# Kernel tuning notes

Measured on AMD Instinct MI355X. Metric: run time of the kernel, lower is better.

## Reference

```python
import jax, jax.numpy as jnp
import numpy as np
import math

N_HEADS = 16

def _ln(x, g, b, eps=1e-5):
    m = jnp.mean(x, axis=-1, keepdims=True)
    v = jnp.var(x, axis=-1, keepdims=True)
    return (x - m) * jax.lax.rsqrt(v + eps) * g + b

def _block(x, ln1_g, ln1_b, ln2_g, ln2_b, wqkv, wo, w1, w2):
    b, k, d = x.shape
    dh = d // N_HEADS
    h = _ln(x, ln1_g, ln1_b)
    qkv = (h @ wqkv).reshape(b, k, 3, N_HEADS, dh)
    q, kk, v = qkv[:, :, 0], qkv[:, :, 1], qkv[:, :, 2]
    scores = jnp.einsum('bqhd,bkhd->bhqk', q, kk) / math.sqrt(dh)
    attn = jax.nn.softmax(scores, axis=-1)
    o = jnp.einsum('bhqk,bkhd->bqhd', attn, v).reshape(b, k, d) @ wo
    x = x + o
    h2 = _ln(x, ln2_g, ln2_b)
    return x + jax.nn.gelu(h2 @ w1) @ w2

def setup_inputs() -> dict:
    key = jax.random.key(0)
    ks = jax.random.split(key, 6)
    b, s, d, dff = 4, 4096, 1024, 4096
    sc = 0.02
    return {
        'x': jax.random.normal(ks[0], (b, s, d), jnp.float32),
        'router_w': jax.random.normal(ks[1], (d,), jnp.float32) * sc,
        'ln1_g': jnp.ones((d,), jnp.float32),
        'ln1_b': jnp.zeros((d,), jnp.float32),
        'ln2_g': jnp.ones((d,), jnp.float32),
        'ln2_b': jnp.zeros((d,), jnp.float32),
        'wqkv': jax.random.normal(ks[2], (d, 3 * d), jnp.float32) * sc,
        'wo': jax.random.normal(ks[3], (d, d), jnp.float32) * sc,
        'w1': jax.random.normal(ks[4], (d, dff), jnp.float32) * sc,
        'w2': jax.random.normal(ks[5], (dff, d), jnp.float32) * sc,
    }

def reference(x, router_w, ln1_g, ln1_b, ln2_g, ln2_b, wqkv, wo, w1, w2):
    b, s, d = x.shape
    K = s // 2  # top_k = int(s * capacity_factor), capacity_factor = 0.5
    logits = x @ router_w                      # [b, s]
    w, idx = jax.lax.top_k(logits, K)          # [b, K]
    order = jnp.argsort(idx, axis=1)           # sort selected tokens by position
    sel = jnp.take_along_axis(idx, order, axis=1)          # [b, K] sorted indices
    fx = jnp.take_along_axis(x, sel[..., None], axis=1)    # gather routed tokens [b, K, d]
    xo = _block(fx, ln1_g, ln1_b, ln2_g, ln2_b, wqkv, wo, w1, w2)
    rw = jnp.take_along_axis(jax.nn.softmax(w, axis=1), order, axis=1)[..., None]  # [b, K, 1]
    batch_idx = jnp.arange(b)[:, None]
    out = x.at[batch_idx, sel].add(rw * xo)    # softmax-weighted scatter-add
    return out
```

## Files before the change

kernel.cpp:

```cpp
#include <hip/hip_runtime.h>
#include <hip/hip_bf16.h>
#include <stdint.h>

typedef __hip_bfloat16 bf16;
typedef __attribute__((ext_vector_type(8))) short short8;
typedef __attribute__((ext_vector_type(4))) float f32x4;
typedef __attribute__((ext_vector_type(2))) unsigned uint2v;
typedef __attribute__((ext_vector_type(4))) unsigned uint4v;
typedef __attribute__((ext_vector_type(4))) unsigned short ushort4v;

#define B_   4
#define S_   4096
#define D_   1024
#define KSEL 2048
#define DFF  4096
#define NH   16
#define DH   64

static __device__ __forceinline__ void load_lds16(const void* g, void* l) {
  __builtin_amdgcn_global_load_lds((const __attribute__((address_space(1))) void*)g,
                                   (__attribute__((address_space(3))) void*)l,
                                   16, 0, 0);
}

static __device__ __forceinline__ short8 scale8(short8 v, float s) {
  short8 r;
#pragma unroll
  for (int i = 0; i < 8; ++i) {
    unsigned u = ((unsigned)(unsigned short)v[i]) << 16;
    float f = __uint_as_float(u) * s;
    bf16 o = __float2bfloat16(f);
    short t;
    __builtin_memcpy(&t, &o, 2);
    r[i] = t;
  }
  return r;
}

static __device__ __forceinline__ unsigned cvt_pk_bf16(float lo, float hi) {
  unsigned r;
  asm("v_cvt_pk_bf16_f32 %0, %1, %2" : "=v"(r) : "v"(lo), "v"(hi));
  return r;
}

static __device__ __forceinline__ void pl32_swap(unsigned &a, unsigned &b) {
#if __has_builtin(__builtin_amdgcn_permlane32_swap)
  uint2v r = __builtin_amdgcn_permlane32_swap(a, b, false, false);
  a = r[0]; b = r[1];
#else
  asm("v_permlane32_swap_b32 %0, %1" : "+v"(a), "+v"(b));
#endif
}

static __device__ __forceinline__ void pl16_swap(unsigned &a, unsigned &b) {
#if __has_builtin(__builtin_amdgcn_permlane16_swap)
  uint2v r = __builtin_amdgcn_permlane16_swap(a, b, false, false);
  a = r[0]; b = r[1];
#else
  asm("v_permlane16_swap_b32 %0, %1" : "+v"(a), "+v"(b));
#endif
}

__global__ __launch_bounds__(256)
void copy_router(const float* __restrict__ x, const float* __restrict__ rwts,
                 float* __restrict__ out, float* __restrict__ logits)
{
  int s = blockIdx.x, b = blockIdx.y;
  int tid = threadIdx.x;
  const float4* row = (const float4*)(x + ((size_t)b * S_ + s) * D_);
  float4 v = row[tid];
  ((float4*)(out + ((size_t)b * S_ + s) * D_))[tid] = v;
  float4 rv = ((const float4*)rwts)[tid];
  float p = v.x * rv.x + v.y * rv.y + v.z * rv.z + v.w * rv.w;
  for (int off = 32; off; off >>= 1) p += __shfl_down(p, off, 64);
  __shared__ float wsum[4];
  if ((tid & 63) == 0) wsum[tid >> 6] = p;
  __syncthreads();
  if (tid == 0) logits[(size_t)b * S_ + s] = wsum[0] + wsum[1] + wsum[2] + wsum[3];
}

__global__ __launch_bounds__(1024)
void topk_kernel(const float* __restrict__ logits,
                 int* __restrict__ sel, float* __restrict__ rw)
{
  __shared__ float lg[4096];
  __shared__ unsigned long long keys[4096];
  __shared__ unsigned char flags[4096];
  __shared__ float wsum[16];
  __shared__ int wtot[16];
  __shared__ int woff[17];

  int b = blockIdx.x, tid = threadIdx.x;
  const float* L = logits + (size_t)b * S_;
  for (int i = tid; i < 4096; i += 1024) {
    float v = L[i];
    lg[i] = v;
    unsigned u = __float_as_uint(v);
    u = (u & 0x80000000u) ? ~u : (u | 0x80000000u);
    u = ~u;
    keys[i] = ((unsigned long long)u << 32) | (unsigned)i;
  }
  __syncthreads();
  for (int k = 2; k <= 4096; k <<= 1) {
    for (int j = k >> 1; j > 0; j >>= 1) {
      for (int t = tid; t < 4096; t += 1024) {
        int ixj = t ^ j;
        if (ixj > t) {
          bool up = ((t & k) == 0);
          unsigned long long a = keys[t], c = keys[ixj];
          if ((a > c) == up) { keys[t] = c; keys[ixj] = a; }
        }
      }
      __syncthreads();
    }
  }
  for (int i = tid; i < 4096; i += 1024) flags[i] = 0;
  __syncthreads();
  for (int i = tid; i < KSEL; i += 1024) flags[(int)(keys[i] & 0xFFFFFFFFu)] = 1;
  __syncthreads();
  float m = lg[(int)(keys[0] & 0xFFFFFFFFu)];
  float part = 0.f;
  for (int i = tid; i < KSEL; i += 1024) part += __expf(lg[(int)(keys[i] & 0xFFFFFFFFu)] - m);
  for (int off = 32; off; off >>= 1) part += __shfl_down(part, off, 64);
  if ((tid & 63) == 0) wsum[tid >> 6] = part;
  __syncthreads();
  if (tid == 0) { float t = 0; for (int w = 0; w < 16; ++w) t += wsum[w]; wsum[0] = t; }
  __syncthreads();
  float inv = 1.0f / wsum[0];
  int base = tid * 4;
  int f0 = flags[base], f1 = flags[base + 1], f2 = flags[base + 2], f3 = flags[base + 3];
  int mysum = f0 + f1 + f2 + f3;
  int incl = mysum;
  int lane = tid & 63;
  for (int off = 1; off < 64; off <<= 1) {
    int t = __shfl_up(incl, off, 64);
    if (lane >= off) incl += t;
  }
  if (lane == 63) wtot[tid >> 6] = incl;
  __syncthreads();
  if (tid == 0) { int sacc = 0; for (int w = 0; w < 16; ++w) { woff[w] = sacc; sacc += wtot[w]; } woff[16] = sacc; }
  __syncthreads();
  int p = woff[tid >> 6] + incl - mysum;
  int fl[4] = { f0, f1, f2, f3 };
  for (int q = 0; q < 4; ++q) {
    if (fl[q]) {
      int idx = base + q;
      sel[b * KSEL + p] = idx;
      rw[b * KSEL + p] = __expf(lg[idx] - m) * inv;
      p++;
    }
  }
}

__global__ __launch_bounds__(256)
void ln_kernel(const float* __restrict__ in, const float* __restrict__ x,
               const int* __restrict__ sel,
               const float* __restrict__ g, const float* __restrict__ beta,
               bf16* __restrict__ out, int gather)
{
  int r = blockIdx.x;
  int tid = threadIdx.x;
  const float* src;
  if (gather) {
    int b = r >> 11, t = r & 2047;
    src = x + ((size_t)b * S_ + sel[b * KSEL + t]) * D_;
  } else {
    src = in + (size_t)r * D_;
  }
  float4 v = ((const float4*)src)[tid];
  float s = v.x + v.y + v.z + v.w;
  float sq = v.x * v.x + v.y * v.y + v.z * v.z + v.w * v.w;
  for (int off = 32; off; off >>= 1) { s += __shfl_down(s, off, 64); sq += __shfl_down(sq, off, 64); }
  __shared__ float wsA[4], wsB[4];
  if ((tid & 63) == 0) { wsA[tid >> 6] = s; wsB[tid >> 6] = sq; }
  __syncthreads();
  float stot = wsA[0] + wsA[1] + wsA[2] + wsA[3];
  float sqt  = wsB[0] + wsB[1] + wsB[2] + wsB[3];
  float mean = stot * (1.f / 1024.f);
  float var  = sqt * (1.f / 1024.f) - mean * mean;
  float rs = rsqrtf(var + 1e-5f);
  float4 gv = ((const float4*)g)[tid];
  float4 bv = ((const float4*)beta)[tid];
  bf16* o = out + (size_t)r * D_ + tid * 4;
  o[0] = __float2bfloat16((v.x - mean) * rs * gv.x + bv.x);
  o[1] = __float2bfloat16((v.y - mean) * rs * gv.y + bv.y);
  o[2] = __float2bfloat16((v.z - mean) * rs * gv.z + bv.z);
  o[3] = __float2bfloat16((v.w - mean) * rs * gv.w + bv.w);
}

__global__ __launch_bounds__(256)
void wtrans(const float* __restrict__ in, bf16* __restrict__ out, int K, int N)
{
  __shared__ float tile[32][33];
  int n0 = blockIdx.x * 32, k0 = blockIdx.y * 32;
  int r = threadIdx.x >> 5, c = threadIdx.x & 31;
#pragma unroll
  for (int i = 0; i < 4; ++i)
    tile[r + 8 * i][c] = in[(size_t)(k0 + r + 8 * i) * N + n0 + c];
  __syncthreads();
#pragma unroll
  for (int i = 0; i < 4; ++i)
    out[(size_t)(n0 + r + 8 * i) * K + k0 + c] = __float2bfloat16(tile[c][r + 8 * i]);
}

__global__ __launch_bounds__(256)
void vt_transpose(const bf16* __restrict__ qkv, bf16* __restrict__ vt)
{
  __shared__ bf16 tile[32][33];
  int bh = blockIdx.z;
  int d0 = blockIdx.y * 32;
  int t0 = blockIdx.x * 32;
  int b = bh >> 4, h = bh & 15;
  int r = threadIdx.x >> 5, c = threadIdx.x & 31;
#pragma unroll
  for (int i = 0; i < 4; ++i) {
    int t = t0 + r + 8 * i;
    tile[r + 8 * i][c] = qkv[(size_t)(b * KSEL + t) * 3072 + 2048 + h * 64 + d0 + c];
  }
  __syncthreads();
#pragma unroll
  for (int i = 0; i < 4; ++i) {
    int d = d0 + r + 8 * i;
    vt[((size_t)bh * 64 + d) * KSEL + t0 + c] = tile[c][r + 8 * i];
  }
}

template<int EPI, int TN>
__global__ __launch_bounds__(256)
void gemm_bt(const bf16* __restrict__ A, const bf16* __restrict__ Bt,
             float* __restrict__ Cf, bf16* __restrict__ Cb,
             int M, int N, int K,
             const float* __restrict__ xin, const int* __restrict__ sel,
             const float* __restrict__ rw, const float* __restrict__ x1,
             float* __restrict__ outp)
{
  constexpr int NT = TN / 32;
  constexpr int WN = TN / 2;
  __shared__ bf16 As[128 * 64];
  __shared__ bf16 Bs[TN * 64];
  const int tid = threadIdx.x;
  const int wid = tid >> 6;
  const int lane = tid & 63;
  const int l15 = lane & 15;
  const int quad = lane >> 4;
  const int wm = wid >> 1, wn = wid & 1;
  const int bm = blockIdx.x * 128;
  const int bn = blockIdx.y * TN;

  const int srow = lane >> 3;
  const int sgrp = (lane & 7) ^ srow;

  f32x4 acc[4][NT] = {};

  for (int k0 = 0; k0 < K; k0 += 64) {
#pragma unroll
    for (int c2 = 0; c2 < 4; ++c2) {
      int c = wid * 4 + c2;
      const bf16* ga = A + (size_t)(bm + c * 8 + srow) * K + (k0 + sgrp * 8);
      load_lds16(ga, &As[c * 512]);
    }
#pragma unroll
    for (int c2 = 0; c2 < TN / 32; ++c2) {
      int c = wid * (TN / 32) + c2;
      const bf16* gb = Bt + (size_t)(bn + c * 8 + srow) * K + (k0 + sgrp * 8);
      load_lds16(gb, &Bs[c * 512]);
    }
    __syncthreads();
#pragma unroll
    for (int ks = 0; ks < 2; ++ks) {
      short8 af[4], bfv[NT];
#pragma unroll
      for (int mt = 0; mt < 4; ++mt) {
        int row = wm * 64 + mt * 16 + l15;
        int cg = (ks * 4 + quad) ^ (row & 7);
        af[mt] = *(const short8*)&As[row * 64 + cg * 8];
      }
#pragma unroll
      for (int nt = 0; nt < NT; ++nt) {
        int row = wn * WN + nt * 16 + l15;
        int cg = (ks * 4 + quad) ^ (row & 7);
        bfv[nt] = *(const short8*)&Bs[row * 64 + cg * 8];
      }
#pragma unroll
      for (int mt = 0; mt < 4; ++mt)
#pragma unroll
        for (int nt = 0; nt < NT; ++nt)
          acc[mt][nt] = __builtin_amdgcn_mfma_f32_16x16x32_bf16(af[mt], bfv[nt], acc[mt][nt], 0, 0, 0);
    }
    __syncthreads();
  }

#pragma unroll
  for (int mt = 0; mt < 4; ++mt) {
#pragma unroll
    for (int r = 0; r < 4; ++r) {
      int gm = bm + wm * 64 + mt * 16 + quad * 4 + r;
      int bb = gm >> 11, tt = gm & 2047;
      int sr = 0; float rwv = 0.f;
      if (EPI == 1 || EPI == 3) sr = sel[bb * KSEL + tt];
      if (EPI == 3) rwv = rw[bb * KSEL + tt];
#pragma unroll
      for (int nt = 0; nt < NT; ++nt) {
        int gn = bn + wn * WN + nt * 16 + l15;
        float v = acc[mt][nt][r];
        if (EPI == 0) {
          Cb[(size_t)gm * N + gn] = __float2bfloat16(v);
        } else if (EPI == 1) {
          float xv = xin[((size_t)bb * S_ + sr) * D_ + gn];
          Cf[(size_t)gm * N + gn] = xv + v;
        } else if (EPI == 2) {
          float u = v;
          float cc = 0.7978845608028654f * (u + 0.044715f * u * u * u);
          float e = __expf(2.f * cc);
          float th = 1.f - 2.f / (e + 1.f);
          Cb[(size_t)gm * N + gn] = __float2bfloat16(0.5f * u * (1.f + th));
        } else {
          float v2 = rwv * (x1[(size_t)gm * D_ + gn] + v);
          outp[((size_t)bb * S_ + sr) * D_ + gn] += v2;
        }
      }
    }
  }
}

__global__ __launch_bounds__(256)
void flash_kernel(const bf16* __restrict__ qkv, const bf16* __restrict__ vt,
                  bf16* __restrict__ attn_o)
{
  __shared__ bf16 Ks[128 * 64];
  __shared__ bf16 Vs[64 * 128];
  int qt = blockIdx.x, h = blockIdx.y, b = blockIdx.z;
  int tid = threadIdx.x, wid = tid >> 6, lane = tid & 63;
  int l15 = lane & 15, quad = lane >> 4;
  int q0 = qt * 128 + wid * 32;

  const int srowK = lane >> 3, sgK = lane & 7;
  const int srowV = lane >> 4, sgV = lane & 15;

  short8 qf[2][2];
#pragma unroll
  for (int mt = 0; mt < 2; ++mt)
#pragma unroll
    for (int ks = 0; ks < 2; ++ks) {
      const bf16* p = qkv + (size_t)(b * KSEL + q0 + mt * 16 + l15) * 3072 + h * 64 + ks * 32 + quad * 8;
      qf[mt][ks] = scale8(*(const short8*)p, 0.125f * 1.44269504f);
    }

  f32x4 acc_ot[2][4] = {};
  float lsum[2] = {};

  const bf16* Vg = vt + (size_t)(b * NH + h) * 64 * KSEL;

  for (int kt = 0; kt < KSEL / 128; ++kt) {
    int tok0 = b * KSEL + kt * 128;
    __syncthreads();
#pragma unroll
    for (int i = 0; i < 4; ++i) {
      int c = wid * 4 + i;
      const bf16* ga = qkv + (size_t)(tok0 + c * 8 + srowK) * 3072 + 1024 + h * 64 + ((sgK ^ srowK) * 8);
      load_lds16(ga, &Ks[c * 512]);
      int vr = c * 4 + srowV;
      const bf16* gv = Vg + (size_t)vr * KSEL + kt * 128 + ((sgV ^ (vr & 7)) * 8);
      load_lds16(gv, &Vs[c * 512]);
    }
    __syncthreads();

#pragma unroll
    for (int ks4 = 0; ks4 < 4; ++ks4) {
      f32x4 s[2][2] = {};
#pragma unroll
      for (int u = 0; u < 2; ++u) {
        int row = (ks4 * 2 + u) * 16 + l15;
#pragma unroll
        for (int ks = 0; ks < 2; ++ks) {
          int g = (ks * 4 + quad) ^ (row & 7);
          short8 kf = *(const short8*)&Ks[row * 64 + g * 8];
#pragma unroll
          for (int mt = 0; mt < 2; ++mt)
            s[mt][u] = __builtin_amdgcn_mfma_f32_16x16x32_bf16(kf, qf[mt][ks], s[mt][u], 0, 0, 0);
        }
      }
      short8 pfrag[2];
#pragma unroll
      for (int mt = 0; mt < 2; ++mt) {
        float pA[4], pB[4];
#pragma unroll
        for (int r = 0; r < 4; ++r) {
          pA[r] = __builtin_amdgcn_exp2f(s[mt][0][r]);
          pB[r] = __builtin_amdgcn_exp2f(s[mt][1][r]);
          lsum[mt] += pA[r] + pB[r];
        }
        unsigned A0 = cvt_pk_bf16(pA[0], pA[1]);
        unsigned A1 = cvt_pk_bf16(pA[2], pA[3]);
        unsigned B0 = cvt_pk_bf16(pB[0], pB[1]);
        unsigned B1 = cvt_pk_bf16(pB[2], pB[3]);
        pl32_swap(A0, B0); pl16_swap(A0, B0);
        pl32_swap(A1, B1); pl16_swap(A1, B1);
        uint4v w; w[0] = A0; w[1] = A1; w[2] = B0; w[3] = B1;
        pfrag[mt] = __builtin_bit_cast(short8, w);
      }
#pragma unroll
      for (int dt = 0; dt < 4; ++dt) {
        int row = dt * 16 + l15;
        int g = (ks4 * 4 + quad) ^ (row & 7);
        short8 vf = *(const short8*)&Vs[row * 128 + g * 8];
#pragma unroll
        for (int mt = 0; mt < 2; ++mt)
          acc_ot[mt][dt] = __builtin_amdgcn_mfma_f32_16x16x32_bf16(vf, pfrag[mt], acc_ot[mt][dt], 0, 0, 0);
      }
    }
  }
#pragma unroll
  for (int mt = 0; mt < 2; ++mt) {
    float l = lsum[mt];
    l += __shfl_xor(l, 16, 64);
    l += __shfl_xor(l, 32, 64);
    float invl = 1.0f / l;
#pragma unroll
    for (int dt = 0; dt < 4; ++dt) {
      ushort4v o;
#pragma unroll
      for (int r = 0; r < 4; ++r) {
        bf16 t = __float2bfloat16(acc_ot[mt][dt][r] * invl);
        unsigned short us;
        __builtin_memcpy(&us, &t, 2);
        o[r] = us;
      }
      *(ushort4v*)(attn_o + (size_t)(b * KSEL + q0 + mt * 16 + l15) * D_ + h * 64 + dt * 16 + quad * 4) = o;
    }
  }
}

extern "C" void kernel_launch(void* const* d_in, const int* in_sizes, int n_in,
                              void* d_out, int out_size, void* d_ws, size_t ws_size,
                              hipStream_t stream)
{
  const float* x      = (const float*)d_in[0];
  const float* router = (const float*)d_in[1];
  const float* ln1g   = (const float*)d_in[2];
  const float* ln1b   = (const float*)d_in[3];
  const float* ln2g   = (const float*)d_in[4];
  const float* ln2b   = (const float*)d_in[5];
  const float* wqkv   = (const float*)d_in[6];
  const float* wo     = (const float*)d_in[7];
  const float* w1     = (const float*)d_in[8];
  const float* w2     = (const float*)d_in[9];
  float* out = (float*)d_out;
  char* ws = (char*)d_ws;

  float* logits = (float*)(ws + 0);
  int*   sel    = (int*)  (ws + 65536);
  float* rw     = (float*)(ws + 98304);
  bf16* wqkvT   = (bf16*) (ws + 131072);
  bf16* woT     = (bf16*) (ws + 6422528);
  bf16* w1T     = (bf16*) (ws + 8519680);
  bf16* w2T     = (bf16*) (ws + 16908288);
  bf16* regA    = (bf16*) (ws + 25296896);
  bf16* regB    = (bf16*) (ws + 42074112);
  bf16* vtb     = (bf16*) (ws + 42074112 + 50331648);
  float* x1     = (float*)(ws + 109182976);

  copy_router<<<dim3(S_, B_), 256, 0, stream>>>(x, router, out, logits);
  topk_kernel<<<B_, 1024, 0, stream>>>(logits, sel, rw);

  wtrans<<<dim3(3072 / 32, 1024 / 32), 256, 0, stream>>>(wqkv, wqkvT, 1024, 3072);
  wtrans<<<dim3(1024 / 32, 1024 / 32), 256, 0, stream>>>(wo,   woT,   1024, 1024);
  wtrans<<<dim3(4096 / 32, 1024 / 32), 256, 0, stream>>>(w1,   w1T,   1024, 4096);
  wtrans<<<dim3(1024 / 32, 4096 / 32), 256, 0, stream>>>(w2,   w2T,   4096, 1024);

  ln_kernel<<<B_ * KSEL, 256, 0, stream>>>(nullptr, x, sel, ln1g, ln1b, regA, 1);

  gemm_bt<0, 128><<<dim3(64, 24), 256, 0, stream>>>(regA, wqkvT, nullptr, regB, 8192, 3072, 1024,
                                                    nullptr, nullptr, nullptr, nullptr, nullptr);
  vt_transpose<<<dim3(KSEL / 32, 2, B_ * NH), 256, 0, stream>>>(regB, vtb);
  flash_kernel<<<dim3(KSEL / 128, NH, B_), 256, 0, stream>>>(regB, vtb, regA);

  gemm_bt<1, 64><<<dim3(64, 16), 256, 0, stream>>>(regA, woT, x1, nullptr, 8192, 1024, 1024,
                                                   x, sel, nullptr, nullptr, nullptr);
  ln_kernel<<<B_ * KSEL, 256, 0, stream>>>(x1, nullptr, nullptr, ln2g, ln2b, regA, 0);
  gemm_bt<2, 128><<<dim3(64, 32), 256, 0, stream>>>(regA, w1T, nullptr, regB, 8192, 4096, 1024,
                                                    nullptr, nullptr, nullptr, nullptr, nullptr);
  gemm_bt<3, 64><<<dim3(64, 16), 256, 0, stream>>>(regB, w2T, nullptr, nullptr, 8192, 1024, 4096,
                                                   nullptr, sel, rw, x1, out);
}
```

Before: 645.7 us.

## Radix-select top-k, double-buffer flash K/V tiles, widen output GEMM tiles

The top-k kernel swaps its full 4096-element bitonic sort for a 32-pass bitwise radix threshold search over register-held keys. Ties at the threshold are broken by position through a prefix scan, and the max is computed by reduction. The flash attention kernel double-buffers its K/V LDS tiles so the next tile's global-to-LDS load is issued before the current tile is computed. The Wo and W2 GEMMs move to 128-wide N tiles with half the grid. Costs are twice the LDS in flash, fewer blocks for the output GEMMs, and tie ordering that differs from the sort-based selection.

```diff
diff --git a/kernel.cpp b/kernel.cpp
--- a/kernel.cpp
+++ b/kernel.cpp
@@ -83,70 +83,91 @@
 void topk_kernel(const float* __restrict__ logits,
                  int* __restrict__ sel, float* __restrict__ rw)
 {
-  __shared__ float lg[4096];
-  __shared__ unsigned long long keys[4096];
-  __shared__ unsigned char flags[4096];
-  __shared__ float wsum[16];
-  __shared__ int wtot[16];
-  __shared__ int woff[17];
+  __shared__ int   wredi[16];
+  __shared__ float wredf[16];
+  __shared__ int   woff[17];
 
   int b = blockIdx.x, tid = threadIdx.x;
+  int lane = tid & 63, wv = tid >> 6;
   const float* L = logits + (size_t)b * S_;
-  for (int i = tid; i < 4096; i += 1024) {
-    float v = L[i];
-    lg[i] = v;
-    unsigned u = __float_as_uint(v);
-    u = (u & 0x80000000u) ? ~u : (u | 0x80000000u);
-    u = ~u;
-    keys[i] = ((unsigned long long)u << 32) | (unsigned)i;
-  }
-  __syncthreads();
-  for (int k = 2; k <= 4096; k <<= 1) {
-    for (int j = k >> 1; j > 0; j >>= 1) {
-      for (int t = tid; t < 4096; t += 1024) {
-        int ixj = t ^ j;
-        if (ixj > t) {
-          bool up = ((t & k) == 0);
-          unsigned long long a = keys[t], c = keys[ixj];
-          if ((a > c) == up) { keys[t] = c; keys[ixj] = a; }
-        }
-      }
-      __syncthreads();
-    }
-  }
-  for (int i = tid; i < 4096; i += 1024) flags[i] = 0;
-  __syncthreads();
-  for (int i = tid; i < KSEL; i += 1024) flags[(int)(keys[i] & 0xFFFFFFFFu)] = 1;
-  __syncthreads();
-  float m = lg[(int)(keys[0] & 0xFFFFFFFFu)];
+  int base = tid * 4;
+  float4 v = ((const float4*)L)[tid];
+  unsigned k0, k1, k2, k3;
+  {
+    unsigned u;
+    u = __float_as_uint(v.x); k0 = (u & 0x80000000u) ? ~u : (u | 0x80000000u);
+    u = __float_as_uint(v.y); k1 = (u & 0x80000000u) ? ~u : (u | 0x80000000u);
+    u = __float_as_uint(v.z); k2 = (u & 0x80000000u) ? ~u : (u | 0x80000000u);
+    u = __float_as_uint(v.w); k3 = (u & 0x80000000u) ? ~u : (u | 0x80000000u);
+  }
+  float mx = fmaxf(fmaxf(v.x, v.y), fmaxf(v.z, v.w));
+  for (int off = 32; off; off >>= 1) mx = fmaxf(mx, __shfl_xor(mx, off, 64));
+  if (lane == 0) wredf[wv] = mx;
+  __syncthreads();
+  float m = wredf[0];
+  for (int w = 1; w < 16; ++w) m = fmaxf(m, wredf[w]);
+
+  unsigned T = 0;
+  for (int bit = 31; bit >= 0; --bit) {
+    unsigned cand = T | (1u << bit);
+    int c = (int)(k0 >= cand) + (int)(k1 >= cand) + (int)(k2 >= cand) + (int)(k3 >= cand);
+    for (int off = 32; off; off >>= 1) c += __shfl_xor(c, off, 64);
+    __syncthreads();
+    if (lane == 0) wredi[wv] = c;
+    __syncthreads();
+    int tot = 0;
+    for (int w = 0; w < 16; ++w) tot += wredi[w];
+    if (tot >= KSEL) T = cand;
+  }
+  int cg = (int)(k0 > T) + (int)(k1 > T) + (int)(k2 > T) + (int)(k3 > T);
+  for (int off = 32; off; off >>= 1) cg += __shfl_xor(cg, off, 64);
+  __syncthreads();
+  if (lane == 0) wredi[wv] = cg;
+  __syncthreads();
+  int n_gt = 0;
+  for (int w = 0; w < 16; ++w) n_gt += wredi[w];
+  int need = KSEL - n_gt;
+  int e0 = (k0 == T), e1 = (k1 == T), e2 = (k2 == T), e3 = (k3 == T);
+  int esum = e0 + e1 + e2 + e3;
+  int eincl = esum;
+  for (int off = 1; off < 64; off <<= 1) { int t = __shfl_up(eincl, off, 64); if (lane >= off) eincl += t; }
+  __syncthreads();
+  if (lane == 63) wredi[wv] = eincl;
+  __syncthreads();
+  int ebase = 0;
+  for (int w = 0; w < wv; ++w) ebase += wredi[w];
+  int ep = ebase + eincl - esum;
+  int f0 = (k0 > T) || (e0 && ep < need); ep += e0;
+  int f1 = (k1 > T) || (e1 && ep < need); ep += e1;
+  int f2 = (k2 > T) || (e2 && ep < need); ep += e2;
+  int f3 = (k3 > T) || (e3 && ep < need); ep += e3;
   float part = 0.f;
-  for (int i = tid; i < KSEL; i += 1024) part += __expf(lg[(int)(keys[i] & 0xFFFFFFFFu)] - m);
-  for (int off = 32; off; off >>= 1) part += __shfl_down(part, off, 64);
-  if ((tid & 63) == 0) wsum[tid >> 6] = part;
-  __syncthreads();
-  if (tid == 0) { float t = 0; for (int w = 0; w < 16; ++w) t += wsum[w]; wsum[0] = t; }
-  __syncthreads();
-  float inv = 1.0f / wsum[0];
-  int base = tid * 4;
-  int f0 = flags[base], f1 = flags[base + 1], f2 = flags[base + 2], f3 = flags[base + 3];
+  if (f0) part += __expf(v.x - m);
+  if (f1) part += __expf(v.y - m);
+  if (f2) part += __expf(v.z - m);
+  if (f3) part += __expf(v.w - m);
+  for (int off = 32; off; off >>= 1) part += __shfl_xor(part, off, 64);
+  __syncthreads();
+  if (lane == 0) wredf[wv] = part;
+  __syncthreads();
+  float tot = 0.f;
+  for (int w = 0; w < 16; ++w) tot += wredf[w];
+  float inv = 1.0f / tot;
   int mysum = f0 + f1 + f2 + f3;
   int incl = mysum;
-  int lane = tid & 63;
-  for (int off = 1; off < 64; off <<= 1) {
-    int t = __shfl_up(incl, off, 64);
-    if (lane >= off) incl += t;
-  }
-  if (lane == 63) wtot[tid >> 6] = incl;
-  __syncthreads();
-  if (tid == 0) { int sacc = 0; for (int w = 0; w < 16; ++w) { woff[w] = sacc; sacc += wtot[w]; } woff[16] = sacc; }
-  __syncthreads();
-  int p = woff[tid >> 6] + incl - mysum;
-  int fl[4] = { f0, f1, f2, f3 };
+  for (int off = 1; off < 64; off <<= 1) { int t = __shfl_up(incl, off, 64); if (lane >= off) incl += t; }
+  __syncthreads();
+  if (lane == 63) wredi[wv] = incl;
+  __syncthreads();
+  if (tid == 0) { int s = 0; for (int w = 0; w < 16; ++w) { woff[w] = s; s += wredi[w]; } woff[16] = s; }
+  __syncthreads();
+  int p = woff[wv] + incl - mysum;
+  float vv[4] = { v.x, v.y, v.z, v.w };
+  int ff[4] = { f0, f1, f2, f3 };
   for (int q = 0; q < 4; ++q) {
-    if (fl[q]) {
-      int idx = base + q;
-      sel[b * KSEL + p] = idx;
-      rw[b * KSEL + p] = __expf(lg[idx] - m) * inv;
+    if (ff[q]) {
+      sel[b * KSEL + p] = base + q;
+      rw[b * KSEL + p] = __expf(vv[q] - m) * inv;
       p++;
     }
   }
@@ -327,8 +348,8 @@
 void flash_kernel(const bf16* __restrict__ qkv, const bf16* __restrict__ vt,
                   bf16* __restrict__ attn_o)
 {
-  __shared__ bf16 Ks[128 * 64];
-  __shared__ bf16 Vs[64 * 128];
+  __shared__ bf16 Ks[2][128 * 64];
+  __shared__ bf16 Vs[2][64 * 128];
   int qt = blockIdx.x, h = blockIdx.y, b = blockIdx.z;
   int tid = threadIdx.x, wid = tid >> 6, lane = tid & 63;
   int l15 = lane & 15, quad = lane >> 4;
@@ -351,19 +372,34 @@
 
   const bf16* Vg = vt + (size_t)(b * NH + h) * 64 * KSEL;
 
-  for (int kt = 0; kt < KSEL / 128; ++kt) {
-    int tok0 = b * KSEL + kt * 128;
-    __syncthreads();
+  {
+    int tok0 = b * KSEL;
 #pragma unroll
     for (int i = 0; i < 4; ++i) {
       int c = wid * 4 + i;
       const bf16* ga = qkv + (size_t)(tok0 + c * 8 + srowK) * 3072 + 1024 + h * 64 + ((sgK ^ srowK) * 8);
-      load_lds16(ga, &Ks[c * 512]);
+      load_lds16(ga, &Ks[0][c * 512]);
       int vr = c * 4 + srowV;
-      const bf16* gv = Vg + (size_t)vr * KSEL + kt * 128 + ((sgV ^ (vr & 7)) * 8);
-      load_lds16(gv, &Vs[c * 512]);
-    }
-    __syncthreads();
+      const bf16* gv = Vg + (size_t)vr * KSEL + ((sgV ^ (vr & 7)) * 8);
+      load_lds16(gv, &Vs[0][c * 512]);
+    }
+  }
+  __syncthreads();
+
+  for (int kt = 0; kt < KSEL / 128; ++kt) {
+    const int cur = kt & 1;
+    if (kt < KSEL / 128 - 1) {
+      int tok0 = b * KSEL + (kt + 1) * 128;
+#pragma unroll
+      for (int i = 0; i < 4; ++i) {
+        int c = wid * 4 + i;
+        const bf16* ga = qkv + (size_t)(tok0 + c * 8 + srowK) * 3072 + 1024 + h * 64 + ((sgK ^ srowK) * 8);
+        load_lds16(ga, &Ks[cur ^ 1][c * 512]);
+        int vr = c * 4 + srowV;
+        const bf16* gv = Vg + (size_t)vr * KSEL + (kt + 1) * 128 + ((sgV ^ (vr & 7)) * 8);
+        load_lds16(gv, &Vs[cur ^ 1][c * 512]);
+      }
+    }
 
 #pragma unroll
     for (int ks4 = 0; ks4 < 4; ++ks4) {
@@ -374,7 +410,7 @@
 #pragma unroll
         for (int ks = 0; ks < 2; ++ks) {
           int g = (ks * 4 + quad) ^ (row & 7);
-          short8 kf = *(const short8*)&Ks[row * 64 + g * 8];
+          short8 kf = *(const short8*)&Ks[cur][row * 64 + g * 8];
 #pragma unroll
           for (int mt = 0; mt < 2; ++mt)
             s[mt][u] = __builtin_amdgcn_mfma_f32_16x16x32_bf16(kf, qf[mt][ks], s[mt][u], 0, 0, 0);
@@ -403,13 +439,15 @@
       for (int dt = 0; dt < 4; ++dt) {
         int row = dt * 16 + l15;
         int g = (ks4 * 4 + quad) ^ (row & 7);
-        short8 vf = *(const short8*)&Vs[row * 128 + g * 8];
+        short8 vf = *(const short8*)&Vs[cur][row * 128 + g * 8];
 #pragma unroll
         for (int mt = 0; mt < 2; ++mt)
           acc_ot[mt][dt] = __builtin_amdgcn_mfma_f32_16x16x32_bf16(vf, pfrag[mt], acc_ot[mt][dt], 0, 0, 0);
       }
     }
-  }
+    __syncthreads();
+  }
+
 #pragma unroll
   for (int mt = 0; mt < 2; ++mt) {
     float l = lsum[mt];
@@ -475,11 +513,11 @@
   vt_transpose<<<dim3(KSEL / 32, 2, B_ * NH), 256, 0, stream>>>(regB, vtb);
   flash_kernel<<<dim3(KSEL / 128, NH, B_), 256, 0, stream>>>(regB, vtb, regA);
 
-  gemm_bt<1, 64><<<dim3(64, 16), 256, 0, stream>>>(regA, woT, x1, nullptr, 8192, 1024, 1024,
+  gemm_bt<1, 128><<<dim3(64, 8), 256, 0, stream>>>(regA, woT, x1, nullptr, 8192, 1024, 1024,
                                                    x, sel, nullptr, nullptr, nullptr);
   ln_kernel<<<B_ * KSEL, 256, 0, stream>>>(x1, nullptr, nullptr, ln2g, ln2b, regA, 0);
   gemm_bt<2, 128><<<dim3(64, 32), 256, 0, stream>>>(regA, w1T, nullptr, regB, 8192, 4096, 1024,
                                                     nullptr, nullptr, nullptr, nullptr, nullptr);
-  gemm_bt<3, 64><<<dim3(64, 16), 256, 0, stream>>>(regB, w2T, nullptr, nullptr, 8192, 1024, 4096,
+  gemm_bt<3, 128><<<dim3(64, 8), 256, 0, stream>>>(regB, w2T, nullptr, nullptr, 8192, 1024, 4096,
                                                    nullptr, sel, rw, x1, out);
 }
```

New measurement: 612.5 us. 5.1% less time.
